# Kernel tuning notes

Hardware: AMD Instinct MI355X
Metric: run time of the kernel (lower is better)

## Reference

```python
import jax, jax.numpy as jnp
import numpy as np

B, N, C, H = 8, 1024, 512, 8
EPS = 1e-6


def setup_inputs() -> dict:
    key = jax.random.key(0)
    k0, k1, k2, k3, k4 = jax.random.split(key, 5)
    x = jax.random.normal(k0, (B, N, C), dtype=jnp.float32)
    # nonnegative random-walk visit-frequency mask stand-in
    mask = jax.random.uniform(k1, (N, N), dtype=jnp.float32)
    w_qkv = jax.random.normal(k2, (C, 3 * C), dtype=jnp.float32) * 0.02
    w_out = jax.random.normal(k3, (C, C), dtype=jnp.float32) * 0.02
    b_out = jax.random.normal(k4, (C,), dtype=jnp.float32) * 0.02
    return {"x": x, "mask": mask, "w_qkv": w_qkv, "w_out": w_out, "b_out": b_out}


def reference(x, mask, w_qkv, w_out, b_out):
    b, n, c = x.shape
    d = c // H
    qkv = x @ w_qkv                                   # [B,N,3C]
    q, k, v = jnp.split(qkv, 3, axis=-1)

    def to_heads(t):
        return t.reshape(b, n, H, d).transpose(0, 2, 1, 3)  # [B,H,N,D]

    q, k, v = to_heads(q), to_heads(k), to_heads(v)
    # positive feature map
    q = jax.nn.relu(q) + EPS
    k = jax.nn.relu(k) + EPS
    # graph diffusion: (q^T @ mask)^T == einsum over source node m
    q = q + 0.1 * jnp.einsum('bhmd,mn->bhnd', q, mask)
    k = k + 0.1 * jnp.einsum('bhmd,mn->bhnd', k, mask)
    # linear kernel scores, elementwise-masked
    kernel = jnp.einsum('bhnd,bhmd->bhnm', q, k) * mask   # [B,H,N,N]
    z = 1.0 / (kernel.sum(axis=-1, keepdims=True) + EPS)  # [B,H,N,1]
    out = jnp.einsum('bhnm,bhmd->bhnd', kernel, v) * z    # [B,H,N,D]
    out = out.transpose(0, 2, 1, 3).reshape(b, n, c)      # [B,N,C]
    return out @ w_out + b_out
```

## Files before the change

### kernel.cpp

```cpp
#include <hip/hip_runtime.h>
#include <cstddef>

#define Bsz 8
#define Nn  1024
#define Cc  512
#define Hh  8
#define Dd  64
#define EPSF 1e-6f

typedef __attribute__((ext_vector_type(8))) short short8;
typedef __attribute__((ext_vector_type(4))) float floatx4;
typedef __attribute__((ext_vector_type(16))) float floatx16;

static __device__ __forceinline__ short f2bf(float f) {
    union { float f; unsigned u; } v; v.f = f;
    unsigned r = (v.u + 0x7FFFu + ((v.u >> 16) & 1u)) >> 16;
    return (short)r;
}
static __device__ __forceinline__ float bf2f(short s) {
    union { unsigned u; float f; } v; v.u = ((unsigned)(unsigned short)s) << 16;
    return v.f;
}

#define GLOAD_LDS16(gp, lp)                                              \
    __builtin_amdgcn_global_load_lds(                                    \
        (const __attribute__((address_space(1))) void*)(gp),             \
        (__attribute__((address_space(3))) void*)(lp), 16, 0, 0)

static __device__ __forceinline__
void stage_tile(short* __restrict__ lds, const short* __restrict__ src,
                int ldsrc, int tid, int CHUNKS, int SLOTS) {
    #pragma unroll
    for (int s = tid; s < SLOTS; s += 256) {
        int r = s / CHUNKS, cs = s % CHUNKS;
        int gc = cs ^ (r & 7);
        GLOAD_LDS16(&src[(size_t)r * ldsrc + gc * 8], &lds[s * 8]);
    }
}
static __device__ __forceinline__
short8 fragT(const short* __restrict__ lds, int CHUNKS, int r, int lc) {
    return *(const short8*)&lds[(r * CHUNKS + (lc ^ (r & 7))) * 8];
}

#define FENCE() asm volatile("" ::: "memory")
#define BARRIER_RAW() do { FENCE(); __builtin_amdgcn_s_barrier(); FENCE(); } while (0)
#define WAITVM(N) asm volatile("s_waitcnt vmcnt(" #N ")" ::: "memory")

__global__ __launch_bounds__(256)
void prep_all(const float* __restrict__ x, const float* __restrict__ mask,
              const float* __restrict__ wq, const float* __restrict__ wo,
              short* __restrict__ xb, short* __restrict__ Ad,
              short* __restrict__ wqT, short* __restrict__ woT,
              short* __restrict__ mbf) {
    __shared__ float t[64][65];
    const int tid = threadIdx.x;
    const int bid = blockIdx.x;

    if (bid < 2048) {
        int idx = bid * 256 + tid;
        const float* s = &x[(size_t)idx * 8];
        union { short h[8]; int4 v; } u;
        #pragma unroll
        for (int j = 0; j < 8; j++) u.h[j] = f2bf(s[j]);
        *(int4*)&xb[(size_t)idx * 8] = u.v;
        return;
    }
    if (bid < 2304) {
        int idx = bid - 2048;
        const int n0 = (idx & 15) * 64, m0 = (idx >> 4) * 64;
        #pragma unroll
        for (int i = 0; i < 4; i++) {
            int k = i * 256 + tid;
            int r = k >> 4, c4 = (k & 15) * 4;
            *(float4*)&t[r][c4] = *(const float4*)&mask[(size_t)(m0 + r) * Nn + n0 + c4];
        }
        __syncthreads();
        #pragma unroll
        for (int i = 0; i < 4; i++) {
            int k = i * 256 + tid;
            int rr = k >> 4, c4 = (k & 15) * 4;
            union { short h[4]; int2 v; } u;
            #pragma unroll
            for (int j = 0; j < 4; j++) {
                int mm = c4 + j;
                float v = 0.1f * t[mm][rr] + ((n0 + rr) == (m0 + mm) ? 1.0f : 0.0f);
                u.h[j] = f2bf(v);
            }
            *(int2*)&Ad[(size_t)(n0 + rr) * Nn + m0 + c4] = u.v;
        }
        return;
    }
    if (bid < 2496) {
        int idx = bid - 2304;
        const int n0 = (idx % 24) * 64, k0 = (idx / 24) * 64;
        #pragma unroll
        for (int i = 0; i < 4; i++) {
            int k = i * 256 + tid;
            int r = k >> 4, c4 = (k & 15) * 4;
            *(float4*)&t[r][c4] = *(const float4*)&wq[(size_t)(k0 + r) * 1536 + n0 + c4];
        }
        __syncthreads();
        #pragma unroll
        for (int i = 0; i < 4; i++) {
            int k = i * 256 + tid;
            int rr = k >> 4, c4 = (k & 15) * 4;
            union { short h[4]; int2 v; } u;
            #pragma unroll
            for (int j = 0; j < 4; j++) u.h[j] = f2bf(t[c4 + j][rr]);
            *(int2*)&wqT[(size_t)(n0 + rr) * 512 + k0 + c4] = u.v;
        }
        return;
    }
    if (bid < 2560) {
        int idx = bid - 2496;
        const int n0 = (idx & 7) * 64, k0 = (idx >> 3) * 64;
        #pragma unroll
        for (int i = 0; i < 4; i++) {
            int k = i * 256 + tid;
            int r = k >> 4, c4 = (k & 15) * 4;
            *(float4*)&t[r][c4] = *(const float4*)&wo[(size_t)(k0 + r) * 512 + n0 + c4];
        }
        __syncthreads();
        #pragma unroll
        for (int i = 0; i < 4; i++) {
            int k = i * 256 + tid;
            int rr = k >> 4, c4 = (k & 15) * 4;
            union { short h[4]; int2 v; } u;
            #pragma unroll
            for (int j = 0; j < 4; j++) u.h[j] = f2bf(t[c4 + j][rr]);
            *(int2*)&woT[(size_t)(n0 + rr) * 512 + k0 + c4] = u.v;
        }
        return;
    }
    {
        int idx = (bid - 2560) * 256 + tid;
        const float* s = &mask[(size_t)idx * 8];
        union { short h[8]; int4 v; } u;
        #pragma unroll
        for (int j = 0; j < 8; j++) u.h[j] = f2bf(s[j]);
        *(int4*)&mbf[(size_t)idx * 8] = u.v;
    }
}

static __device__ __forceinline__
void stageA_half(short* __restrict__ buf, const short* __restrict__ gA,
                 int kt, int h, int tid) {
    #pragma unroll
    for (int kk = 0; kk < 2; kk++) {
        int i = tid + kk * 512;
        int run = i >> 9;
        int within = i & 511;
        int r = run * 128 + h * 64 + (within >> 3);
        int c = within & 7;
        int gc = c ^ (r & 7);
        GLOAD_LDS16(gA + (size_t)r * 512 + kt + gc * 8, buf + (r * 8 + c) * 8);
    }
}
static __device__ __forceinline__
void stageB_half(short* __restrict__ buf, const short* __restrict__ gB,
                 int kt, int h, int tid) {
    #pragma unroll
    for (int kk = 0; kk < 2; kk++) {
        int i = tid + kk * 512;
        int run = i >> 8;
        int within = i & 255;
        int r = run * 64 + h * 32 + (within >> 3);
        int c = within & 7;
        int gc = c ^ (r & 7);
        GLOAD_LDS16(gB + (size_t)r * 512 + kt + gc * 8, buf + (r * 8 + c) * 8);
    }
}

template<int MH>
static __device__ __forceinline__
void readA8(const short* __restrict__ bufA, short8 (&aF)[4][2],
            int wr, int l16, int quad) {
    #pragma unroll
    for (int f = 0; f < 4; f++)
        #pragma unroll
        for (int kk = 0; kk < 2; kk++)
            aF[f][kk] = fragT(bufA, 8, wr * 128 + MH * 64 + f * 16 + l16, kk * 4 + quad);
}
template<int NH>
static __device__ __forceinline__
void readB4(const short* __restrict__ bufB, short8 (&bF)[2][2],
            int wc, int l16, int quad) {
    #pragma unroll
    for (int g = 0; g < 2; g++)
        #pragma unroll
        for (int kk = 0; kk < 2; kk++)
            bF[g][kk] = fragT(bufB, 8, wc * 64 + NH * 32 + g * 16 + l16, kk * 4 + quad);
}
template<int MH, int NH>
static __device__ __forceinline__
void mfma16(short8 (&aF)[4][2], short8 (&bF)[2][2], floatx4 (&acc)[8][4]) {
    #pragma unroll
    for (int kk = 0; kk < 2; kk++)
        #pragma unroll
        for (int f = 0; f < 4; f++)
            #pragma unroll
            for (int g = 0; g < 2; g++)
                acc[MH * 4 + f][NH * 2 + g] = __builtin_amdgcn_mfma_f32_16x16x32_bf16(
                    aF[f][kk], bF[g][kk], acc[MH * 4 + f][NH * 2 + g], 0, 0, 0);
}

__global__ __launch_bounds__(512, 2)
void gemm_qkv(const short* __restrict__ xb, const short* __restrict__ wqT,
              short* __restrict__ qT, short* __restrict__ kT,
              short* __restrict__ vT) {
    extern __shared__ short smem[];

    const int tid = threadIdx.x;
    const int lin = blockIdx.x;
    const int wgid = (lin & 7) * 24 + (lin >> 3);
    const int mt = wgid / 6, nt = wgid % 6;
    const int m0 = mt * 256, n0 = nt * 256;

    const int wid = tid >> 6, lane = tid & 63;
    const int quad = lane >> 4, l16 = lane & 15;
    const int wr = wid >> 2, wc = wid & 3;

    const short* Ab = xb  + (size_t)m0 * 512;
    const short* Bb = wqT + (size_t)n0 * 512;

    floatx4 acc[8][4];
    #pragma unroll
    for (int i = 0; i < 8; i++)
        #pragma unroll
        for (int j = 0; j < 4; j++) acc[i][j] = (floatx4){0.f, 0.f, 0.f, 0.f};

    short8 aF[4][2], bF[2][2];

    stageA_half(smem,          Ab, 0, 0, tid);
    stageB_half(smem + 16384,  Bb, 0, 0, tid);
    stageA_half(smem,          Ab, 0, 1, tid);
    stageB_half(smem + 16384,  Bb, 0, 1, tid);
    WAITVM(4); BARRIER_RAW();

    for (int j = 0; j < 8; ++j) {
        const short* cA = smem + (j & 1) * 32768;
        const short* cB = cA + 16384;
        short* nA = smem + ((j + 1) & 1) * 32768;
        short* nB = nA + 16384;
        const int kn = ((j + 1) & 7) * 64;

        readA8<0>(cA, aF, wr, l16, quad);
        readB4<0>(cB, bF, wc, l16, quad);
        stageA_half(nA, Ab, kn, 0, tid);
        stageB_half(nB, Bb, kn, 0, tid);
        BARRIER_RAW();
        __builtin_amdgcn_s_setprio(1);
        mfma16<0, 0>(aF, bF, acc);
        __builtin_amdgcn_s_setprio(0);
        WAITVM(4); BARRIER_RAW();

        readA8<1>(cA, aF, wr, l16, quad);
        stageA_half(nA, Ab, kn, 1, tid);
        stageB_half(nB, Bb, kn, 1, tid);
        BARRIER_RAW();
        __builtin_amdgcn_s_setprio(1);
        mfma16<1, 0>(aF, bF, acc);
        __builtin_amdgcn_s_setprio(0);
        BARRIER_RAW();

        readB4<1>(cB, bF, wc, l16, quad);
        BARRIER_RAW();
        __builtin_amdgcn_s_setprio(1);
        mfma16<1, 1>(aF, bF, acc);
        __builtin_amdgcn_s_setprio(0);
        BARRIER_RAW();

        readA8<0>(cA, aF, wr, l16, quad);
        BARRIER_RAW();
        __builtin_amdgcn_s_setprio(1);
        mfma16<0, 1>(aF, bF, acc);
        __builtin_amdgcn_s_setprio(0);
        WAITVM(4); BARRIER_RAW();
    }

    WAITVM(0); BARRIER_RAW();

    short* T = smem + wid * 8192;
    const int doRelu = (n0 < 1024);
    #pragma unroll
    for (int mf = 0; mf < 8; mf++)
        #pragma unroll
        for (int nf = 0; nf < 4; nf++)
            #pragma unroll
            for (int rr = 0; rr < 4; rr++) {
                float v = acc[mf][nf][rr];
                if (doRelu) v = fmaxf(v, 0.0f) + EPSF;
                int row = nf * 16 + l16;
                int col = mf * 16 + quad * 4 + rr;
                T[row * 128 + (col ^ ((row & 15) << 3))] = f2bf(v);
            }
    const int gm0 = m0 + wr * 128;
    const int b = gm0 >> 10, m_in0 = gm0 & 1023;
    #pragma unroll
    for (int g = 0; g < 4; g++) {
        int row = (lane >> 2) + g * 16;
        int gn = n0 + wc * 64 + row;
        int part = gn >> 9, ci = gn & 511;
        short* base = (part == 0) ? qT : (part == 1) ? kT : vT;
        short* dst = base + ((size_t)b * 512 + ci) * 1024 + m_in0;
        #pragma unroll
        for (int cc = 0; cc < 4; cc++) {
            int cs = ((lane & 3) + cc * 4) * 8;
            *(int4*)&dst[cs] = *(const int4*)&T[row * 128 + (cs ^ ((row & 15) << 3))];
        }
    }
}

static __device__ __forceinline__
void dstageA_half(short* __restrict__ buf, const short* __restrict__ gA,
                  int kt, int h, int tid) {
    #pragma unroll
    for (int kk = 0; kk < 2; kk++) {
        int i = tid + kk * 512;
        int rl = i >> 3;
        int c  = i & 7;
        int r  = (rl >> 5) * 64 + h * 32 + (rl & 31);
        int gc = c ^ (r & 7);
        GLOAD_LDS16(gA + (size_t)r * 1024 + kt + gc * 8, buf + (r * 8 + c) * 8);
    }
}
static __device__ __forceinline__
void dstageB_half(short* __restrict__ buf, const short* __restrict__ gB,
                  int kt, int h, int tid) {
    int rl = tid >> 3;
    int c  = tid & 7;
    int r  = (rl >> 5) * 64 + h * 32 + (rl & 31);
    int gc = c ^ (r & 7);
    GLOAD_LDS16(gB + (size_t)r * 1024 + kt + gc * 8, buf + (r * 8 + c) * 8);
}
template<int MH>
static __device__ __forceinline__
void dreadA(const short* __restrict__ bufA, short8 (&aF)[2][2],
            int wr, int l16, int quad) {
    #pragma unroll
    for (int f = 0; f < 2; f++)
        #pragma unroll
        for (int kk = 0; kk < 2; kk++)
            aF[f][kk] = fragT(bufA, 8, wr * 64 + MH * 32 + f * 16 + l16, kk * 4 + quad);
}
template<int NH>
static __device__ __forceinline__
void dreadB(const short* __restrict__ bufB, short8 (&bF)[2][2],
            int wc, int l16, int quad) {
    #pragma unroll
    for (int g = 0; g < 2; g++)
        #pragma unroll
        for (int kk = 0; kk < 2; kk++)
            bF[g][kk] = fragT(bufB, 8, wc * 64 + NH * 32 + g * 16 + l16, kk * 4 + quad);
}
template<int MH, int NH>
static __device__ __forceinline__
void dmfma8(short8 (&aF)[2][2], short8 (&bF)[2][2], floatx4 (&acc)[4][4]) {
    #pragma unroll
    for (int kk = 0; kk < 2; kk++)
        #pragma unroll
        for (int f = 0; f < 2; f++)
            #pragma unroll
            for (int g = 0; g < 2; g++)
                acc[MH * 2 + f][NH * 2 + g] = __builtin_amdgcn_mfma_f32_16x16x32_bf16(
                    aF[f][kk], bF[g][kk], acc[MH * 2 + f][NH * 2 + g], 0, 0, 0);
}

__global__ __launch_bounds__(512, 2)
void gemm_diff8(const short* __restrict__ Ad, const short* __restrict__ qT,
                const short* __restrict__ kT, short* __restrict__ qd,
                short* __restrict__ kd) {
    extern __shared__ short smem[];

    const int tid = threadIdx.x;
    const int lin = blockIdx.x;
    const int wgid = (lin & 7) * 32 + (lin >> 3);
    const int mt = wgid >> 6, ct = wgid & 63;
    const int m0 = mt * 256;
    const int seg = ct >> 2, cb = (ct & 3) * 128;
    const int b = seg >> 1, part = seg & 1;

    const short* Bb = ((part ? kT : qT) + (size_t)b * 512 * 1024) + (size_t)cb * 1024;
    short* outb = (part ? kd : qd) + (size_t)b * 1024 * 512;
    const short* Abase = Ad + (size_t)m0 * 1024;

    const int wid = tid >> 6, lane = tid & 63;
    const int quad = lane >> 4, l16 = lane & 15;
    const int wr = wid >> 1, wc = wid & 1;

    floatx4 acc[4][4];
    #pragma unroll
    for (int i = 0; i < 4; i++)
        #pragma unroll
        for (int j = 0; j < 4; j++) acc[i][j] = (floatx4){0.f, 0.f, 0.f, 0.f};

    short8 aF[2][2], bF[2][2];

    dstageA_half(smem,          Abase, 0, 0, tid);
    dstageB_half(smem + 16384,  Bb,    0, 0, tid);
    dstageA_half(smem,          Abase, 0, 1, tid);
    dstageB_half(smem + 16384,  Bb,    0, 1, tid);
    WAITVM(3); BARRIER_RAW();

    for (int j = 0; j < 16; ++j) {
        const short* cA = smem + (j & 1) * 24576;
        const short* cB = cA + 16384;
        short* nA = smem + ((j + 1) & 1) * 24576;
        short* nB = nA + 16384;
        const int kn = ((j + 1) & 15) * 64;

        dreadA<0>(cA, aF, wr, l16, quad);
        dreadB<0>(cB, bF, wc, l16, quad);
        dstageA_half(nA, Abase, kn, 0, tid);
        dstageB_half(nB, Bb,    kn, 0, tid);
        BARRIER_RAW();
        __builtin_amdgcn_s_setprio(1);
        dmfma8<0, 0>(aF, bF, acc);
        __builtin_amdgcn_s_setprio(0);
        WAITVM(3); BARRIER_RAW();

        dreadA<1>(cA, aF, wr, l16, quad);
        dstageA_half(nA, Abase, kn, 1, tid);
        dstageB_half(nB, Bb,    kn, 1, tid);
        BARRIER_RAW();
        __builtin_amdgcn_s_setprio(1);
        dmfma8<1, 0>(aF, bF, acc);
        __builtin_amdgcn_s_setprio(0);
        BARRIER_RAW();

        dreadB<1>(cB, bF, wc, l16, quad);
        BARRIER_RAW();
        __builtin_amdgcn_s_setprio(1);
        dmfma8<1, 1>(aF, bF, acc);
        __builtin_amdgcn_s_setprio(0);
        BARRIER_RAW();

        dreadA<0>(cA, aF, wr, l16, quad);
        BARRIER_RAW();
        __builtin_amdgcn_s_setprio(1);
        dmfma8<0, 1>(aF, bF, acc);
        __builtin_amdgcn_s_setprio(0);
        WAITVM(3); BARRIER_RAW();
    }
    WAITVM(0);

    #pragma unroll
    for (int fr = 0; fr < 4; fr++)
        #pragma unroll
        for (int rr = 0; rr < 4; rr++) {
            int n = m0 + wr * 64 + fr * 16 + quad * 4 + rr;
            #pragma unroll
            for (int fc = 0; fc < 4; fc++) {
                int c = cb + wc * 64 + fc * 16 + l16;
                outb[(size_t)n * 512 + c] = f2bf(acc[fr][fc][rr]);
            }
        }
}

__global__ __launch_bounds__(256)
void attn_mfma(const short* __restrict__ qd, const short* __restrict__ kd,
               const short* __restrict__ vTg, const short* __restrict__ mbf,
               short* __restrict__ abf) {
    __shared__ short qs[8192];
    __shared__ short ks[4096];
    __shared__ short vt[4096];
    __shared__ short ms[8192];

    const int tid = threadIdx.x;
    const int bh = blockIdx.x;
    const int b = bh >> 3, h = bh & 7;
    const int n0 = blockIdx.y * 128;

    const int wave = tid >> 6, lane = tid & 63;
    const int l32 = lane & 31, hi = lane >> 5;

    const short* Qb = qd + ((size_t)b * Nn + n0) * Cc + h * Dd;
    const short* Kb = kd + (size_t)b * Nn * Cc + h * Dd;
    const short* Vb = vTg + ((size_t)b * Cc + h * Dd) * Nn;
    const short* Mb = mbf + (size_t)n0 * Nn;

    stage_tile(qs, Qb, Cc, tid, 8, 1024);
    __syncthreads();
    short8 qf[4];
    #pragma unroll
    for (int j = 0; j < 4; j++)
        qf[j] = fragT(qs, 8, wave * 32 + l32, 2 * j + hi);

    float dreg = 0.f;
    floatx16 nacc0, nacc1;
    #pragma unroll
    for (int i = 0; i < 16; i++) { nacc0[i] = 0.f; nacc1[i] = 0.f; }

    for (int m0 = 0; m0 < Nn; m0 += 64) {
        __syncthreads();
        stage_tile(ks, Kb + (size_t)m0 * Cc, Cc, tid, 8, 512);
        stage_tile(vt, Vb + m0, Nn, tid, 8, 512);
        stage_tile(ms, Mb + m0, Nn, tid, 8, 1024);
        __syncthreads();

        #pragma unroll
        for (int msub = 0; msub < 2; msub++) {
            floatx16 S;
            #pragma unroll
            for (int i = 0; i < 16; i++) S[i] = 0.f;
            #pragma unroll
            for (int j = 0; j < 4; j++) {
                const short8 kf = fragT(ks, 8, msub * 32 + l32, 2 * j + hi);
                S = __builtin_amdgcn_mfma_f32_32x32x16_bf16(kf, qf[j], S, 0, 0, 0);
            }
            const int mrow = wave * 32 + l32;
            float sv[16];
            int w[8];
            #pragma unroll
            for (int g = 0; g < 4; g++) {
                const int c = msub * 4 + g;
                const int off = (mrow * 8 + (c ^ (mrow & 7))) * 8 + hi * 4;
                union { short hh[4]; int2 v; } mk;
                mk.v = *(const int2*)&ms[off];
                #pragma unroll
                for (int ri = 0; ri < 4; ri++) {
                    float s = S[4 * g + ri] * bf2f(mk.hh[ri]);
                    sv[4 * g + ri] = s;
                    dreg += s;
                }
                int wl, wh;
                asm("v_cvt_pk_bf16_f32 %0, %1, %2"
                    : "=v"(wl) : "v"(sv[4 * g]), "v"(sv[4 * g + 1]));
                asm("v_cvt_pk_bf16_f32 %0, %1, %2"
                    : "=v"(wh) : "v"(sv[4 * g + 2]), "v"(sv[4 * g + 3]));
                w[2 * g] = wl; w[2 * g + 1] = wh;
            }
            int sx[8];
            #pragma unroll
            for (int i = 0; i < 8; i++) sx[i] = __shfl_xor(w[i], 32, 64);
            union { int wi[4]; short8 v; } pa0, pa1;
            pa0.wi[0] = hi ? sx[2] : w[0];
            pa0.wi[1] = hi ? sx[3] : w[1];
            pa0.wi[2] = hi ? w[2]  : sx[0];
            pa0.wi[3] = hi ? w[3]  : sx[1];
            pa1.wi[0] = hi ? sx[6] : w[4];
            pa1.wi[1] = hi ? sx[7] : w[5];
            pa1.wi[2] = hi ? w[6]  : sx[4];
            pa1.wi[3] = hi ? w[7]  : sx[5];
            __builtin_amdgcn_s_setprio(1);
            {
                const short8 v00 = fragT(vt, 8, 0 * 32 + l32, msub * 4 + 0 + hi);
                const short8 v01 = fragT(vt, 8, 0 * 32 + l32, msub * 4 + 2 + hi);
                nacc0 = __builtin_amdgcn_mfma_f32_32x32x16_bf16(pa0.v, v00, nacc0, 0, 0, 0);
                nacc0 = __builtin_amdgcn_mfma_f32_32x32x16_bf16(pa1.v, v01, nacc0, 0, 0, 0);
                const short8 v10 = fragT(vt, 8, 1 * 32 + l32, msub * 4 + 0 + hi);
                const short8 v11 = fragT(vt, 8, 1 * 32 + l32, msub * 4 + 2 + hi);
                nacc1 = __builtin_amdgcn_mfma_f32_32x32x16_bf16(pa0.v, v10, nacc1, 0, 0, 0);
                nacc1 = __builtin_amdgcn_mfma_f32_32x32x16_bf16(pa1.v, v11, nacc1, 0, 0, 0);
            }
            __builtin_amdgcn_s_setprio(0);
        }
    }

    dreg += __shfl_xor(dreg, 32, 64);

    float den16[16];
    #pragma unroll
    for (int g = 0; g < 4; g++)
        #pragma unroll
        for (int ri = 0; ri < 4; ri++)
            den16[4 * g + ri] = __shfl(dreg, 8 * g + 4 * hi + ri, 64);

    #pragma unroll
    for (int g = 0; g < 4; g++)
        #pragma unroll
        for (int ri = 0; ri < 4; ri++) {
            const int nl = 8 * g + 4 * hi + ri;
            const int n = n0 + wave * 32 + nl;
            const float zr = 1.0f / (den16[4 * g + ri] + EPSF);
            size_t o = ((size_t)b * Nn + n) * Cc + h * Dd + l32;
            abf[o]      = f2bf(nacc0[4 * g + ri] * zr);
            abf[o + 32] = f2bf(nacc1[4 * g + ri] * zr);
        }
}

__global__ __launch_bounds__(256)
void gemm_out(const short* __restrict__ abf, const short* __restrict__ woT,
              const float* __restrict__ bias, float* __restrict__ out) {
    __shared__ short smem[12288];
    short* As = smem;
    short* Bs = smem + 4096;

    const int tid = threadIdx.x;
    const int m0 = blockIdx.y * 64;
    const int n0 = blockIdx.x * 128;
    const int wave = tid >> 6, lane = tid & 63;
    const int quad = lane >> 4, l16 = lane & 15;
    const int wm = (wave >> 1) * 32, wn = (wave & 1) * 64;

    floatx4 acc[2][4];
    #pragma unroll
    for (int i = 0; i < 2; i++)
        #pragma unroll
        for (int j = 0; j < 4; j++) acc[i][j] = (floatx4){0.f, 0.f, 0.f, 0.f};

    const short* Ab = abf + (size_t)m0 * 512;
    const short* Bb = woT + (size_t)n0 * 512;

    for (int k0 = 0; k0 < 512; k0 += 64) {
        __syncthreads();
        stage_tile(As, Ab + k0, 512, tid, 8, 512);
        stage_tile(Bs, Bb + k0, 512, tid, 8, 1024);
        __syncthreads();
        #pragma unroll
        for (int kh = 0; kh < 2; kh++) {
            short8 a[2], b[4];
            #pragma unroll
            for (int i = 0; i < 2; i++)
                a[i] = fragT(As, 8, wm + i * 16 + l16, kh * 4 + quad);
            #pragma unroll
            for (int i = 0; i < 4; i++)
                b[i] = fragT(Bs, 8, wn + i * 16 + l16, kh * 4 + quad);
            #pragma unroll
            for (int mi = 0; mi < 2; mi++)
                #pragma unroll
                for (int ni = 0; ni < 4; ni++)
                    acc[mi][ni] = __builtin_amdgcn_mfma_f32_16x16x32_bf16(
                        a[mi], b[ni], acc[mi][ni], 0, 0, 0);
        }
    }

    #pragma unroll
    for (int mi = 0; mi < 2; mi++)
        #pragma unroll
        for (int r = 0; r < 4; r++) {
            int m = m0 + wm + mi * 16 + quad * 4 + r;
            #pragma unroll
            for (int ni = 0; ni < 4; ni++) {
                int n = n0 + wn + ni * 16 + l16;
                out[(size_t)m * 512 + n] = acc[mi][ni][r] + bias[n];
            }
        }
}

extern "C" void kernel_launch(void* const* d_in, const int* in_sizes, int n_in,
                              void* d_out, int out_size, void* d_ws, size_t ws_size,
                              hipStream_t stream) {
    const float* x     = (const float*)d_in[0];
    const float* mask  = (const float*)d_in[1];
    const float* w_qkv = (const float*)d_in[2];
    const float* w_out = (const float*)d_in[3];
    const float* b_out = (const float*)d_in[4];
    float* out = (float*)d_out;

    char* p = (char*)d_ws;
    short* xb  = (short*)p; p += 8388608;
    short* wqT = (short*)p; p += 1572864;
    short* Ad  = (short*)p; p += 2097152;
    short* woT = (short*)p; p += 524288;
    short* mbf = (short*)p; p += 2097152;
    short* qT  = (short*)p; p += 8388608;
    short* kT  = (short*)p; p += 8388608;
    short* vT  = (short*)p; p += 8388608;
    short* qd  = (short*)p; p += 8388608;
    short* kd  = (short*)p; p += 8388608;
    short* abf = (short*)p; p += 8388608;

    static int attr_set = 0;
    if (!attr_set) {
        hipFuncSetAttribute(reinterpret_cast<const void*>(gemm_qkv),
                            hipFuncAttributeMaxDynamicSharedMemorySize, 131072);
        hipFuncSetAttribute(reinterpret_cast<const void*>(gemm_diff8),
                            hipFuncAttributeMaxDynamicSharedMemorySize, 98304);
        attr_set = 1;
    }

    dim3 blk(256);

    prep_all  <<<3072, blk, 0, stream>>>(x, mask, w_qkv, w_out,
                                         xb, Ad, wqT, woT, mbf);
    gemm_qkv  <<<dim3(192), dim3(512), 131072, stream>>>(xb, wqT, qT, kT, vT);
    gemm_diff8<<<dim3(256), dim3(512), 98304, stream>>>(Ad, qT, kT, qd, kd);
    attn_mfma <<<dim3(64, 8),  blk, 0, stream>>>(qd, kd, vT, mbf, abf);
    gemm_out  <<<dim3(4, 128), blk, 0, stream>>>(abf, woT, b_out, out);
}
```

Measured before the change: 169.0 us.

## Load mask fragments directly to registers with double-buffered prefetch

Stops staging the mask tile through LDS. Each lane now reads its own mask elements from global memory into registers, one 64-column tile ahead, alternating between two register sets so the load overlaps the current tile's MFMA work. This removes the LDS stores and loads for the mask and frees shared memory. In exchange it adds register pressure and uses narrow, uncoalesced 8-byte global reads per lane instead of cooperative staged loads.

```diff
diff --git a/kernel.cpp b/kernel.cpp
--- a/kernel.cpp
+++ b/kernel.cpp
@@ -457,6 +457,66 @@
         }
 }
 
+static __device__ __forceinline__
+void attn_tile32(const short* __restrict__ ks, const short* __restrict__ vt,
+                 const int2 (&M)[2][4], const short8 (&qf)[4],
+                 float& dreg, floatx16& nacc0, floatx16& nacc1,
+                 int l32, int hi) {
+    #pragma unroll
+    for (int msub = 0; msub < 2; msub++) {
+        floatx16 S;
+        #pragma unroll
+        for (int i = 0; i < 16; i++) S[i] = 0.f;
+        #pragma unroll
+        for (int j = 0; j < 4; j++) {
+            const short8 kf = fragT(ks, 8, msub * 32 + l32, 2 * j + hi);
+            S = __builtin_amdgcn_mfma_f32_32x32x16_bf16(kf, qf[j], S, 0, 0, 0);
+        }
+        float sv[16];
+        int w[8];
+        #pragma unroll
+        for (int g = 0; g < 4; g++) {
+            union { short hh[4]; int2 v; } mk; mk.v = M[msub][g];
+            #pragma unroll
+            for (int ri = 0; ri < 4; ri++) {
+                float s = S[4 * g + ri] * bf2f(mk.hh[ri]);
+                sv[4 * g + ri] = s;
+                dreg += s;
+            }
+            int wl, wh;
+            asm("v_cvt_pk_bf16_f32 %0, %1, %2"
+                : "=v"(wl) : "v"(sv[4 * g]), "v"(sv[4 * g + 1]));
+            asm("v_cvt_pk_bf16_f32 %0, %1, %2"
+                : "=v"(wh) : "v"(sv[4 * g + 2]), "v"(sv[4 * g + 3]));
+            w[2 * g] = wl; w[2 * g + 1] = wh;
+        }
+        int sx[8];
+        #pragma unroll
+        for (int i = 0; i < 8; i++) sx[i] = __shfl_xor(w[i], 32, 64);
+        union { int wi[4]; short8 v; } pa0, pa1;
+        pa0.wi[0] = hi ? sx[2] : w[0];
+        pa0.wi[1] = hi ? sx[3] : w[1];
+        pa0.wi[2] = hi ? w[2]  : sx[0];
+        pa0.wi[3] = hi ? w[3]  : sx[1];
+        pa1.wi[0] = hi ? sx[6] : w[4];
+        pa1.wi[1] = hi ? sx[7] : w[5];
+        pa1.wi[2] = hi ? w[6]  : sx[4];
+        pa1.wi[3] = hi ? w[7]  : sx[5];
+        __builtin_amdgcn_s_setprio(1);
+        {
+            const short8 v00 = fragT(vt, 8, 0 * 32 + l32, msub * 4 + 0 + hi);
+            const short8 v01 = fragT(vt, 8, 0 * 32 + l32, msub * 4 + 2 + hi);
+            nacc0 = __builtin_amdgcn_mfma_f32_32x32x16_bf16(pa0.v, v00, nacc0, 0, 0, 0);
+            nacc0 = __builtin_amdgcn_mfma_f32_32x32x16_bf16(pa1.v, v01, nacc0, 0, 0, 0);
+            const short8 v10 = fragT(vt, 8, 1 * 32 + l32, msub * 4 + 0 + hi);
+            const short8 v11 = fragT(vt, 8, 1 * 32 + l32, msub * 4 + 2 + hi);
+            nacc1 = __builtin_amdgcn_mfma_f32_32x32x16_bf16(pa0.v, v10, nacc1, 0, 0, 0);
+            nacc1 = __builtin_amdgcn_mfma_f32_32x32x16_bf16(pa1.v, v11, nacc1, 0, 0, 0);
+        }
+        __builtin_amdgcn_s_setprio(0);
+    }
+}
+
 __global__ __launch_bounds__(256)
 void attn_mfma(const short* __restrict__ qd, const short* __restrict__ kd,
                const short* __restrict__ vTg, const short* __restrict__ mbf,
@@ -464,7 +524,6 @@
     __shared__ short qs[8192];
     __shared__ short ks[4096];
     __shared__ short vt[4096];
-    __shared__ short ms[8192];
 
     const int tid = threadIdx.x;
     const int bh = blockIdx.x;
@@ -477,9 +536,15 @@
     const short* Qb = qd + ((size_t)b * Nn + n0) * Cc + h * Dd;
     const short* Kb = kd + (size_t)b * Nn * Cc + h * Dd;
     const short* Vb = vTg + ((size_t)b * Cc + h * Dd) * Nn;
-    const short* Mb = mbf + (size_t)n0 * Nn;
+    const short* baseM = mbf + (size_t)(n0 + wave * 32 + l32) * Nn + 4 * hi;
 
     stage_tile(qs, Qb, Cc, tid, 8, 1024);
+    int2 MA[2][4], MB[2][4];
+    #pragma unroll
+    for (int msx = 0; msx < 2; msx++)
+        #pragma unroll
+        for (int g = 0; g < 4; g++)
+            MA[msx][g] = *(const int2*)(baseM + msx * 32 + 8 * g);
     __syncthreads();
     short8 qf[4];
     #pragma unroll
@@ -491,70 +556,31 @@
     #pragma unroll
     for (int i = 0; i < 16; i++) { nacc0[i] = 0.f; nacc1[i] = 0.f; }
 
-    for (int m0 = 0; m0 < Nn; m0 += 64) {
-        __syncthreads();
-        stage_tile(ks, Kb + (size_t)m0 * Cc, Cc, tid, 8, 512);
-        stage_tile(vt, Vb + m0, Nn, tid, 8, 512);
-        stage_tile(ms, Mb + m0, Nn, tid, 8, 1024);
-        __syncthreads();
-
-        #pragma unroll
-        for (int msub = 0; msub < 2; msub++) {
-            floatx16 S;
-            #pragma unroll
-            for (int i = 0; i < 16; i++) S[i] = 0.f;
-            #pragma unroll
-            for (int j = 0; j < 4; j++) {
-                const short8 kf = fragT(ks, 8, msub * 32 + l32, 2 * j + hi);
-                S = __builtin_amdgcn_mfma_f32_32x32x16_bf16(kf, qf[j], S, 0, 0, 0);
-            }
-            const int mrow = wave * 32 + l32;
-            float sv[16];
-            int w[8];
-            #pragma unroll
-            for (int g = 0; g < 4; g++) {
-                const int c = msub * 4 + g;
-                const int off = (mrow * 8 + (c ^ (mrow & 7))) * 8 + hi * 4;
-                union { short hh[4]; int2 v; } mk;
-                mk.v = *(const int2*)&ms[off];
+    for (int jo = 0; jo < 8; jo++) {
+        const int j0 = 2 * jo;
+        __syncthreads();
+        stage_tile(ks, Kb + (size_t)j0 * 64 * Cc, Cc, tid, 8, 512);
+        stage_tile(vt, Vb + j0 * 64,             Nn, tid, 8, 512);
+        __syncthreads();
+        #pragma unroll
+        for (int msx = 0; msx < 2; msx++)
+            #pragma unroll
+            for (int g = 0; g < 4; g++)
+                MB[msx][g] = *(const int2*)(baseM + (j0 + 1) * 64 + msx * 32 + 8 * g);
+        attn_tile32(ks, vt, MA, qf, dreg, nacc0, nacc1, l32, hi);
+
+        __syncthreads();
+        stage_tile(ks, Kb + (size_t)(j0 + 1) * 64 * Cc, Cc, tid, 8, 512);
+        stage_tile(vt, Vb + (j0 + 1) * 64,             Nn, tid, 8, 512);
+        __syncthreads();
+        if (jo < 7) {
+            #pragma unroll
+            for (int msx = 0; msx < 2; msx++)
                 #pragma unroll
-                for (int ri = 0; ri < 4; ri++) {
-                    float s = S[4 * g + ri] * bf2f(mk.hh[ri]);
-                    sv[4 * g + ri] = s;
-                    dreg += s;
-                }
-                int wl, wh;
-                asm("v_cvt_pk_bf16_f32 %0, %1, %2"
-                    : "=v"(wl) : "v"(sv[4 * g]), "v"(sv[4 * g + 1]));
-                asm("v_cvt_pk_bf16_f32 %0, %1, %2"
-                    : "=v"(wh) : "v"(sv[4 * g + 2]), "v"(sv[4 * g + 3]));
-                w[2 * g] = wl; w[2 * g + 1] = wh;
-            }
-            int sx[8];
-            #pragma unroll
-            for (int i = 0; i < 8; i++) sx[i] = __shfl_xor(w[i], 32, 64);
-            union { int wi[4]; short8 v; } pa0, pa1;
-            pa0.wi[0] = hi ? sx[2] : w[0];
-            pa0.wi[1] = hi ? sx[3] : w[1];
-            pa0.wi[2] = hi ? w[2]  : sx[0];
-            pa0.wi[3] = hi ? w[3]  : sx[1];
-            pa1.wi[0] = hi ? sx[6] : w[4];
-            pa1.wi[1] = hi ? sx[7] : w[5];
-            pa1.wi[2] = hi ? w[6]  : sx[4];
-            pa1.wi[3] = hi ? w[7]  : sx[5];
-            __builtin_amdgcn_s_setprio(1);
-            {
-                const short8 v00 = fragT(vt, 8, 0 * 32 + l32, msub * 4 + 0 + hi);
-                const short8 v01 = fragT(vt, 8, 0 * 32 + l32, msub * 4 + 2 + hi);
-                nacc0 = __builtin_amdgcn_mfma_f32_32x32x16_bf16(pa0.v, v00, nacc0, 0, 0, 0);
-                nacc0 = __builtin_amdgcn_mfma_f32_32x32x16_bf16(pa1.v, v01, nacc0, 0, 0, 0);
-                const short8 v10 = fragT(vt, 8, 1 * 32 + l32, msub * 4 + 0 + hi);
-                const short8 v11 = fragT(vt, 8, 1 * 32 + l32, msub * 4 + 2 + hi);
-                nacc1 = __builtin_amdgcn_mfma_f32_32x32x16_bf16(pa0.v, v10, nacc1, 0, 0, 0);
-                nacc1 = __builtin_amdgcn_mfma_f32_32x32x16_bf16(pa1.v, v11, nacc1, 0, 0, 0);
-            }
-            __builtin_amdgcn_s_setprio(0);
-        }
+                for (int g = 0; g < 4; g++)
+                    MA[msx][g] = *(const int2*)(baseM + (j0 + 2) * 64 + msx * 32 + 8 * g);
+        }
+        attn_tile32(ks, vt, MB, qf, dreg, nacc0, nacc1, l32, hi);
     }
 
     dreg += __shfl_xor(dreg, 32, 64);
```

After: 175.4 us. 1.04x slower.
